# Optimization experiments

Measured on AMD Instinct MI355X. Metric: run time of the kernel, lower is better.

Reference implementation:

```python
import jax, jax.numpy as jnp
import numpy as np

DN = ('NCHW', 'OIHW', 'NCHW')
PAD1 = [(1, 1), (1, 1)]


def conv3x3(x, w):
    return jax.lax.conv_general_dilated(x, w, window_strides=(1, 1), padding=PAD1, dimension_numbers=DN)


def setup_inputs() -> dict:
    key = jax.random.key(0)
    ks = jax.random.split(key, 5)
    B, C, H, W = 8, 256, 56, 56
    return {
        'x': jax.random.normal(ks[0], (B, C, H, W), jnp.float32),
        'weight': jax.random.normal(ks[1], (C, C, 3, 3), jnp.float32) * 0.05,
        'A_w': jax.random.normal(ks[2], (1, C, 3, 3), jnp.float32),
        'se_w1': jax.random.normal(ks[3], (16, C, 3, 3), jnp.float32) * 0.02,
        'se_w2': jax.random.normal(ks[4], (1, 16, 3, 3), jnp.float32) * 0.1,
    }


def reference(x, weight, A_w, se_w1, se_w2):
    # weight = weight * A_w (A_w broadcasts over the output-channel dim)
    w = weight * A_w  # [C, C, 3, 3]
    # SE-style spatial attention map A: [B, 1, H, W]
    a = jax.nn.sigmoid(conv3x3(jax.nn.relu(conv3x3(x, se_w1)), se_w2))
    # Torch: unfold(x) * A, then matmul with flattened weight. Since A
    # broadcasts across the C*9 patch dim, this equals conv2d(x, w) * A.
    out = conv3x3(x, w) * a  # [B, C, H, W]
    return out
```

## Files before the change

### kernel.cpp

```cpp
#include <hip/hip_runtime.h>


typedef unsigned short u16;
typedef __bf16 bf16x8 __attribute__((ext_vector_type(8)));
typedef unsigned short us8 __attribute__((ext_vector_type(8)));
typedef unsigned short us4v __attribute__((ext_vector_type(4)));
typedef float f32x4 __attribute__((ext_vector_type(4)));
typedef float f4v __attribute__((ext_vector_type(4)));

#define HP 58
#define HW 3136

__device__ __forceinline__ u16 f2bf(float f) {
  unsigned u = __float_as_uint(f);
  u = (u + 0x7fffu + ((u >> 16) & 1u)) >> 16;
  return (u16)u;
}
__device__ __forceinline__ float bf2f(u16 v) {
  return __uint_as_float(((unsigned)v) << 16);
}

__device__ __forceinline__ void gload16(const u16* g, u16* l) {
  __builtin_amdgcn_global_load_lds((const __attribute__((address_space(1))) void*)g,
                                   (__attribute__((address_space(3))) void*)l,
                                   16, 0, 0);
}

__global__ __launch_bounds__(256) void k_pre(const float* __restrict__ x,
                                             const float* __restrict__ weight,
                                             const float* __restrict__ A_w,
                                             const float* __restrict__ se_w1,
                                             u16* __restrict__ xp, u16* __restrict__ wb,
                                             u16* __restrict__ w1b, u16* __restrict__ se1p) {
  __shared__ __align__(16) u16 trans[56 * 72];
  const int bid = blockIdx.x;
  const int t = threadIdx.x;
  if (bid < 448) {
    const int h = bid % 56, b = bid / 56;
    if (t < 64) {
      int half = t >> 5, seg = t & 31;
      us8 z8 = {};
      *(us8*)(xp + ((size_t)((b * HP + h + 1) * HP + half * 57)) * 256 + seg * 8) = z8;
    }
    for (int cc = 0; cc < 4; ++cc) {
      const int c0 = cc * 64;
#pragma unroll
      for (int i = 0; i < 4; ++i) {
        int idx = t + 256 * i;
        if (idx < 896) {
          int ci = idx / 14, s = idx % 14;
          f4v v = *(const f4v*)(x + ((size_t)(b * 256 + c0 + ci)) * HW + h * 56 + s * 4);
#pragma unroll
          for (int j = 0; j < 4; ++j) trans[(s * 4 + j) * 72 + ci] = f2bf(v[j]);
        }
      }
      __syncthreads();
#pragma unroll
      for (int i = 0; i < 2; ++i) {
        int idx = t + 256 * i;
        if (idx < 448) {
          int w = idx >> 3, seg = idx & 7;
          us8 v = *(const us8*)&trans[w * 72 + seg * 8];
          *(us8*)(xp + ((size_t)((b * HP + h + 1) * HP + (w + 1))) * 256 + c0 + seg * 8) = v;
        }
      }
      __syncthreads();
    }
  } else if (bid < 2896) {
    int idx = (bid - 448) * 256 + t;
    if (idx < 589824) {
      int tap = idx >> 16; int rem = idx & 65535; int o = rem >> 8; int c = rem & 255;
      wb[idx] = f2bf(weight[(o * 256 + c) * 9 + tap] * A_w[c * 9 + tap]);
    } else if (idx < 589824 + 36864) {
      int j = idx - 589824;
      int tap = j >> 12; int rem = j & 4095; int o = rem >> 8; int c = rem & 255;
      w1b[j] = f2bf(se_w1[(o * 256 + c) * 9 + tap]);
    }
  } else {
    int zid = (bid - 2896) * 256 + t;
    us8 z8 = {};
#pragma unroll
    for (int j = 0; j < 2; ++j) {
      int ch = zid + j * 45056;
      if (ch < 29696) {
        int b = ch / 3712; int rem = ch - b * 3712;
        int row = (rem < 1856) ? 0 : 57;
        int r2 = (rem < 1856) ? rem : rem - 1856;
        int col = r2 >> 5, seg = r2 & 31;
        *(us8*)(xp + ((size_t)((b * HP + row) * HP + col)) * 256 + seg * 8) = z8;
      } else if (ch < 29696 + 53824) {
        int c2 = ch - 29696;
        *(us8*)(se1p + (size_t)c2 * 8) = z8;
      }
    }
  }
}

__global__ __launch_bounds__(256) void k_se1(const u16* __restrict__ xp,
                                             const u16* __restrict__ w1b,
                                             u16* __restrict__ se1p) {
  __shared__ __align__(16) u16 Alds[144 * 64];
  __shared__ __align__(16) u16 slab[3 * 64 * 64];
  const int t = threadIdx.x;
  const int lane = t & 63;
  const int wv = t >> 6;
  const int l15 = lane & 15, lg = lane >> 4;
  const int wg = blockIdx.x;
  const int b = wg & 7;
  const int h = wg >> 3;

  f32x4 acc = {0.f, 0.f, 0.f, 0.f};

  for (int cc = 0; cc < 4; ++cc) {
    const int c0 = cc * 64;
    __syncthreads();
    for (int idx = t; idx < 1152; idx += 256) {
      int row = idx >> 3, seg = idx & 7;
      us8 v = *(const us8*)(w1b + ((size_t)row * 256 + c0 + seg * 8));
      *(us8*)&Alds[row * 64 + (seg ^ (row & 7)) * 8] = v;
    }
#pragma unroll
    for (int i = 0; i < 6; ++i) {
      int chunk = i * 256 + t;
      int row = chunk >> 9, col = (chunk >> 3) & 63, seg = chunk & 7;
      const u16* src = xp + ((size_t)((b * HP + h + row) * HP + col)) * 256 + c0 +
                       ((seg ^ (col & 7)) * 8);
      gload16(src, &slab[(i * 256 + wv * 64) * 8]);
    }
    __syncthreads();
#pragma unroll
    for (int tap = 0; tap < 9; ++tap) {
      const int dh = tap / 3, dw = tap % 3;
#pragma unroll
      for (int kk = 0; kk < 2; ++kk) {
        int arow = tap * 16 + l15;
        bf16x8 af = *(const bf16x8*)&Alds[arow * 64 + (((kk * 4 + lg) ^ (arow & 7))) * 8];
        int col = ((wv * 16 + l15) + dw) & 63;
        bf16x8 bfr = *(const bf16x8*)&slab[((dh * 64 + col) * 8 + ((kk * 4 + lg) ^ (col & 7))) * 8];
        acc = __builtin_amdgcn_mfma_f32_16x16x32_bf16(af, bfr, acc, 0, 0, 0);
      }
    }
  }
  int w = wv * 16 + l15;
  if (w < 56) {
    us4v pk;
#pragma unroll
    for (int reg = 0; reg < 4; ++reg) {
      float v = acc[reg];
      v = v > 0.f ? v : 0.f;
      pk[reg] = f2bf(v);
    }
    *(us4v*)(se1p + ((size_t)((b * HP + h + 1) * HP + (w + 1))) * 16 + lg * 4) = pk;
  }
}

__global__ __launch_bounds__(256) void k_main(const u16* __restrict__ xp,
                                              const u16* __restrict__ wb,
                                              const u16* __restrict__ se1p,
                                              const float* __restrict__ se_w2,
                                              float* __restrict__ out) {
  __shared__ __align__(16) u16 S[24576];
  u16* slab  = S;
  u16* Albuf = S + 16384;
  float* w2s    = (float*)S;
  float* amap_s = (float*)(S + 512);
  const int t = threadIdx.x;
  const int lane = t & 63;
  const int wid = t >> 6;
  const int wm = wid >> 1;
  const int wn = wid & 1;
  const int l15 = lane & 15, lg = lane >> 4;
  const int lrow = lane >> 3, lseg = lane & 7;
  const int wg = blockIdx.x;
  const int b = wg & 7;
  const int rem = wg >> 3;
  const int h0 = (rem >> 1) * 2;
  const int mbase = (rem & 1) * 128;

  f32x4 acc[4][4];
#pragma unroll
  for (int mt = 0; mt < 4; ++mt)
#pragma unroll
    for (int nt = 0; nt < 4; ++nt) {
      f32x4 z = {0.f, 0.f, 0.f, 0.f};
      acc[mt][nt] = z;
    }

  auto stage_slab = [&](int cc) {
    const int c0 = cc * 64;
#pragma unroll
    for (int i = 0; i < 8; ++i) {
      int chunk = wid * 512 + i * 64 + lane;
      int row = chunk >> 9, col = (chunk >> 3) & 63, seg = chunk & 7;
      const u16* src = xp + ((size_t)((b * HP + h0 + row) * HP + col)) * 256 + c0 +
                       ((seg ^ (col & 7)) * 8);
      gload16(src, &slab[(wid * 512 + i * 64) * 8]);
    }
  };
  auto loadA = [&](int tap, int cc, us8* ra) {
    const int c0 = cc * 64;
#pragma unroll
    for (int i = 0; i < 4; ++i) {
      int row = wid * 32 + i * 8 + lrow;
      ra[i] = *(const us8*)(wb + ((size_t)(tap * 256 + mbase + row)) * 256 + c0 + lseg * 8);
    }
  };
  auto writeA = [&](const us8* ra) {
#pragma unroll
    for (int i = 0; i < 4; ++i) {
      int row = wid * 32 + i * 8 + lrow;
      *(us8*)&Albuf[row * 64 + (lseg ^ (row & 7)) * 8] = ra[i];
    }
  };

  {
    us8 ra[4];
    loadA(0, 0, ra);
    stage_slab(0);
    writeA(ra);
    __syncthreads();
  }

  for (int cc = 0; cc < 4; ++cc) {
#pragma unroll
    for (int tap = 0; tap < 9; ++tap) {
      const bool haveNext = !(cc == 3 && tap == 8);
      us8 ra[4];
      if (haveNext) loadA(tap < 8 ? tap + 1 : 0, tap < 8 ? cc : cc + 1, ra);
      const int dh = tap / 3, dw = tap % 3;
#pragma unroll
      for (int kk = 0; kk < 2; ++kk) {
        bf16x8 af[4], bfr[4];
#pragma unroll
        for (int mt = 0; mt < 4; ++mt) {
          int row = wm * 64 + mt * 16 + l15;
          af[mt] = *(const bf16x8*)&Albuf[row * 64 + (((kk * 4 + lg) ^ (row & 7))) * 8];
        }
#pragma unroll
        for (int nt = 0; nt < 4; ++nt) {
          int p = wn * 64 + nt * 16 + l15;
          int r = (p >> 6) + dh;
          int col = ((p & 63) + dw) & 63;
          bfr[nt] = *(const bf16x8*)&slab[((r * 64 + col) * 8 + ((kk * 4 + lg) ^ (col & 7))) * 8];
        }
#pragma unroll
        for (int mt = 0; mt < 4; ++mt)
#pragma unroll
          for (int nt = 0; nt < 4; ++nt)
            acc[mt][nt] = __builtin_amdgcn_mfma_f32_16x16x32_bf16(af[mt], bfr[nt], acc[mt][nt], 0, 0, 0);
      }
      __syncthreads();
      if (haveNext) {
        writeA(ra);
        if (tap == 8) stage_slab(cc + 1);
        __syncthreads();
      }
    }
  }

  if (t < 144) w2s[t] = se_w2[t];
  __syncthreads();
  if (t < 112) {
    int r = t / 56, w = t - r * 56;
    int h = h0 + r;
    float s = 0.f;
    for (int dh2 = 0; dh2 < 3; ++dh2) {
#pragma unroll
      for (int dw2 = 0; dw2 < 3; ++dw2) {
        const u16* src = se1p + ((size_t)((b * HP + h + dh2) * HP + (w + dw2))) * 16;
        us8 v0 = *(const us8*)src;
        us8 v1 = *(const us8*)(src + 8);
        int tap = dh2 * 3 + dw2;
#pragma unroll
        for (int ci = 0; ci < 8; ++ci) s += bf2f(v0[ci]) * w2s[ci * 9 + tap];
#pragma unroll
        for (int ci = 0; ci < 8; ++ci) s += bf2f(v1[ci]) * w2s[(8 + ci) * 9 + tap];
      }
    }
    amap_s[t] = 1.f / (1.f + expf(-s));
  }
  __syncthreads();
#pragma unroll
  for (int nt = 0; nt < 4; ++nt) {
    int n = wn * 64 + nt * 16 + l15;
    int r = n >> 6, w = n & 63;
    if (w < 56) {
      float av = amap_s[r * 56 + w];
#pragma unroll
      for (int mt = 0; mt < 4; ++mt) {
        int obase = mbase + wm * 64 + mt * 16 + lg * 4;
#pragma unroll
        for (int reg = 0; reg < 4; ++reg) {
          out[((size_t)(b * 256 + obase + reg) * 56 + h0 + r) * 56 + w] = acc[mt][nt][reg] * av;
        }
      }
    }
  }
}

extern "C" void kernel_launch(void* const* d_in, const int* in_sizes, int n_in,
                              void* d_out, int out_size, void* d_ws, size_t ws_size,
                              hipStream_t stream) {
  const float* x      = (const float*)d_in[0];
  const float* weight = (const float*)d_in[1];
  const float* A_w    = (const float*)d_in[2];
  const float* se_w1  = (const float*)d_in[3];
  const float* se_w2  = (const float*)d_in[4];
  float* out = (float*)d_out;

  char* ws = (char*)d_ws;
  u16* xp   = (u16*)ws;
  u16* se1p = (u16*)(ws + 13778944);
  u16* wb   = (u16*)(ws + 14640128);
  u16* w1b  = (u16*)(ws + 15819776);

  k_pre<<<dim3(3072), dim3(256), 0, stream>>>(x, weight, A_w, se_w1, xp, wb, w1b, se1p);
  k_se1<<<dim3(448), dim3(256), 0, stream>>>(xp, w1b, se1p);
  k_main<<<dim3(448), dim3(256), 0, stream>>>(xp, wb, se1p, se_w2, out);
}
```

Before: 160.3 us.

## Double-buffer weight tiles via direct-to-LDS loads and use 8 waves in main conv

The main conv kernel now runs 512 threads (8 waves, 2x4 wave grid with 4x2 MFMA tiles each). Weight tiles are loaded straight into double-buffered LDS with global_load_lds and waited on with explicit vmcnt, in place of register staging plus a second barrier. MFMA sections also get a raised scheduling priority. The weight-repack prologue is restructured so each thread converts all 9 taps of one (o,c) pair, which shrinks the k_pre grid, and w1b indexing is updated to match. The trade-off is a larger LDS footprint and reliance on hand-written waitcnt counts staying correct.

New measurement: 150.2 us. 1.07x faster.

```diff
diff --git a/kernel.cpp b/kernel.cpp
--- a/kernel.cpp
+++ b/kernel.cpp
@@ -66,18 +66,24 @@
       }
       __syncthreads();
     }
-  } else if (bid < 2896) {
+  } else if (bid < 704) {
     int idx = (bid - 448) * 256 + t;
-    if (idx < 589824) {
-      int tap = idx >> 16; int rem = idx & 65535; int o = rem >> 8; int c = rem & 255;
-      wb[idx] = f2bf(weight[(o * 256 + c) * 9 + tap] * A_w[c * 9 + tap]);
-    } else if (idx < 589824 + 36864) {
-      int j = idx - 589824;
-      int tap = j >> 12; int rem = j & 4095; int o = rem >> 8; int c = rem & 255;
-      w1b[j] = f2bf(se_w1[(o * 256 + c) * 9 + tap]);
+    int o = idx >> 8, c = idx & 255;
+    const float* wsrc = weight + (size_t)idx * 9;
+    const float* asrc = A_w + c * 9;
+#pragma unroll
+    for (int tap = 0; tap < 9; ++tap)
+      wb[tap * 65536 + o * 256 + c] = f2bf(wsrc[tap] * asrc[tap]);
+  } else if (bid < 720) {
+    int idx = (bid - 704) * 256 + t;
+    if (idx < 4096) {
+      const float* wsrc = se_w1 + (size_t)idx * 9;
+#pragma unroll
+      for (int tap = 0; tap < 9; ++tap)
+        w1b[tap * 4096 + idx] = f2bf(wsrc[tap]);
     }
   } else {
-    int zid = (bid - 2896) * 256 + t;
+    int zid = (bid - 720) * 256 + t;
     us8 z8 = {};
 #pragma unroll
     for (int j = 0; j < 2; ++j) {
@@ -116,7 +122,7 @@
     __syncthreads();
     for (int idx = t; idx < 1152; idx += 256) {
       int row = idx >> 3, seg = idx & 7;
-      us8 v = *(const us8*)(w1b + ((size_t)row * 256 + c0 + seg * 8));
+      us8 v = *(const us8*)(w1b + ((size_t)(row / 16) * 4096 + (row & 15) * 256 + c0 + seg * 8));
       *(us8*)&Alds[row * 64 + (seg ^ (row & 7)) * 8] = v;
     }
 #pragma unroll
@@ -154,21 +160,21 @@
   }
 }
 
-__global__ __launch_bounds__(256) void k_main(const u16* __restrict__ xp,
-                                              const u16* __restrict__ wb,
-                                              const u16* __restrict__ se1p,
-                                              const float* __restrict__ se_w2,
-                                              float* __restrict__ out) {
-  __shared__ __align__(16) u16 S[24576];
-  u16* slab  = S;
-  u16* Albuf = S + 16384;
+__global__ __launch_bounds__(512, 4) void k_main(const u16* __restrict__ xp,
+                                                 const u16* __restrict__ wb,
+                                                 const u16* __restrict__ se1p,
+                                                 const float* __restrict__ se_w2,
+                                                 float* __restrict__ out) {
+  __shared__ __align__(16) u16 S[32768];
+  u16* slab = S;
+  u16* Albuf0 = S + 16384;
   float* w2s    = (float*)S;
   float* amap_s = (float*)(S + 512);
   const int t = threadIdx.x;
   const int lane = t & 63;
   const int wid = t >> 6;
-  const int wm = wid >> 1;
-  const int wn = wid & 1;
+  const int wm = wid >> 2;
+  const int wn = wid & 3;
   const int l15 = lane & 15, lg = lane >> 4;
   const int lrow = lane >> 3, lseg = lane & 7;
   const int wg = blockIdx.x;
@@ -177,11 +183,11 @@
   const int h0 = (rem >> 1) * 2;
   const int mbase = (rem & 1) * 128;
 
-  f32x4 acc[4][4];
+  f32x4 acc[4][2];
 #pragma unroll
   for (int mt = 0; mt < 4; ++mt)
 #pragma unroll
-    for (int nt = 0; nt < 4; ++nt) {
+    for (int nt = 0; nt < 2; ++nt) {
       f32x4 z = {0.f, 0.f, 0.f, 0.f};
       acc[mt][nt] = z;
     }
@@ -189,56 +195,55 @@
   auto stage_slab = [&](int cc) {
     const int c0 = cc * 64;
 #pragma unroll
-    for (int i = 0; i < 8; ++i) {
-      int chunk = wid * 512 + i * 64 + lane;
+    for (int i = 0; i < 4; ++i) {
+      int chunk = wid * 256 + i * 64 + lane;
       int row = chunk >> 9, col = (chunk >> 3) & 63, seg = chunk & 7;
       const u16* src = xp + ((size_t)((b * HP + h0 + row) * HP + col)) * 256 + c0 +
                        ((seg ^ (col & 7)) * 8);
-      gload16(src, &slab[(wid * 512 + i * 64) * 8]);
+      gload16(src, &slab[(wid * 256 + i * 64) * 8]);
     }
   };
-  auto loadA = [&](int tap, int cc, us8* ra) {
+  auto stage_A = [&](int tap, int cc, int buf) {
     const int c0 = cc * 64;
-#pragma unroll
-    for (int i = 0; i < 4; ++i) {
-      int row = wid * 32 + i * 8 + lrow;
-      ra[i] = *(const us8*)(wb + ((size_t)(tap * 256 + mbase + row)) * 256 + c0 + lseg * 8);
+    u16* dst = Albuf0 + buf * 8192;
+#pragma unroll
+    for (int i = 0; i < 2; ++i) {
+      int li = wid * 2 + i;
+      int row = li * 8 + lrow;
+      const u16* src = wb + ((size_t)(tap * 256 + mbase + row)) * 256 + c0 +
+                       ((lseg ^ (row & 7)) * 8);
+      gload16(src, &dst[li * 512]);
     }
   };
-  auto writeA = [&](const us8* ra) {
-#pragma unroll
-    for (int i = 0; i < 4; ++i) {
-      int row = wid * 32 + i * 8 + lrow;
-      *(us8*)&Albuf[row * 64 + (lseg ^ (row & 7)) * 8] = ra[i];
-    }
-  };
-
-  {
-    us8 ra[4];
-    loadA(0, 0, ra);
-    stage_slab(0);
-    writeA(ra);
-    __syncthreads();
-  }
-
+
+  stage_slab(0);
+  stage_A(0, 0, 0);
+  int pb = 0;
   for (int cc = 0; cc < 4; ++cc) {
 #pragma unroll
     for (int tap = 0; tap < 9; ++tap) {
-      const bool haveNext = !(cc == 3 && tap == 8);
-      us8 ra[4];
-      if (haveNext) loadA(tap < 8 ? tap + 1 : 0, tap < 8 ? cc : cc + 1, ra);
+      if (tap < 8) {
+        stage_A(tap + 1, cc, pb ^ 1);
+        asm volatile("s_waitcnt vmcnt(2)" ::: "memory");
+      } else {
+        asm volatile("s_waitcnt vmcnt(0)" ::: "memory");
+      }
+      __builtin_amdgcn_s_barrier();
+      __builtin_amdgcn_sched_barrier(0);
       const int dh = tap / 3, dw = tap % 3;
+      const u16* Ab = Albuf0 + pb * 8192;
+      __builtin_amdgcn_s_setprio(1);
 #pragma unroll
       for (int kk = 0; kk < 2; ++kk) {
-        bf16x8 af[4], bfr[4];
+        bf16x8 af[4], bfr[2];
 #pragma unroll
         for (int mt = 0; mt < 4; ++mt) {
           int row = wm * 64 + mt * 16 + l15;
-          af[mt] = *(const bf16x8*)&Albuf[row * 64 + (((kk * 4 + lg) ^ (row & 7))) * 8];
-        }
-#pragma unroll
-        for (int nt = 0; nt < 4; ++nt) {
-          int p = wn * 64 + nt * 16 + l15;
+          af[mt] = *(const bf16x8*)&Ab[row * 64 + (((kk * 4 + lg) ^ (row & 7))) * 8];
+        }
+#pragma unroll
+        for (int nt = 0; nt < 2; ++nt) {
+          int p = wn * 32 + nt * 16 + l15;
           int r = (p >> 6) + dh;
           int col = ((p & 63) + dw) & 63;
           bfr[nt] = *(const bf16x8*)&slab[((r * 64 + col) * 8 + ((kk * 4 + lg) ^ (col & 7))) * 8];
@@ -246,15 +251,17 @@
 #pragma unroll
         for (int mt = 0; mt < 4; ++mt)
 #pragma unroll
-          for (int nt = 0; nt < 4; ++nt)
+          for (int nt = 0; nt < 2; ++nt)
             acc[mt][nt] = __builtin_amdgcn_mfma_f32_16x16x32_bf16(af[mt], bfr[nt], acc[mt][nt], 0, 0, 0);
       }
-      __syncthreads();
-      if (haveNext) {
-        writeA(ra);
-        if (tap == 8) stage_slab(cc + 1);
-        __syncthreads();
-      }
+      __builtin_amdgcn_s_setprio(0);
+      __builtin_amdgcn_sched_barrier(0);
+      __builtin_amdgcn_s_barrier();
+      if (tap == 8 && cc < 3) {
+        stage_slab(cc + 1);
+        stage_A(0, cc + 1, pb ^ 1);
+      }
+      pb ^= 1;
     }
   }
 
@@ -281,8 +288,8 @@
   }
   __syncthreads();
 #pragma unroll
-  for (int nt = 0; nt < 4; ++nt) {
-    int n = wn * 64 + nt * 16 + l15;
+  for (int nt = 0; nt < 2; ++nt) {
+    int n = wn * 32 + nt * 16 + l15;
     int r = n >> 6, w = n & 63;
     if (w < 56) {
       float av = amap_s[r * 56 + w];
@@ -314,7 +321,7 @@
   u16* wb   = (u16*)(ws + 14640128);
   u16* w1b  = (u16*)(ws + 15819776);
 
-  k_pre<<<dim3(3072), dim3(256), 0, stream>>>(x, weight, A_w, se_w1, xp, wb, w1b, se1p);
+  k_pre<<<dim3(896), dim3(256), 0, stream>>>(x, weight, A_w, se_w1, xp, wb, w1b, se1p);
   k_se1<<<dim3(448), dim3(256), 0, stream>>>(xp, w1b, se1p);
-  k_main<<<dim3(448), dim3(256), 0, stream>>>(xp, wb, se1p, se_w2, out);
-}
+  k_main<<<dim3(448), dim3(512), 0, stream>>>(xp, wb, se1p, se_w2, out);
+}
```
